# Optimization experiments

Hardware: AMD Instinct MI355X
Metric: run time of the kernel (lower is better)

## Reference

```python
import jax, jax.numpy as jnp
import numpy as np

B, N, C = 2, 2048, 1024
H = 16
HD = C // H  # 64


def setup_inputs() -> dict:
    key = jax.random.key(0)
    k1, k2, k3 = jax.random.split(key, 3)
    x = jax.random.normal(k1, (B, N, C), dtype=jnp.float32)
    w_qkv = jax.random.normal(k2, (C, 3 * C), dtype=jnp.float32) * (C ** -0.5)
    b_qkv = jnp.zeros((3 * C,), dtype=jnp.float32)
    w_out = jax.random.normal(k3, (C, C), dtype=jnp.float32) * (C ** -0.5)
    b_out = jnp.zeros((C,), dtype=jnp.float32)
    return {"x": x, "w_qkv": w_qkv, "b_qkv": b_qkv, "w_out": w_out, "b_out": b_out}


def reference(x, w_qkv, b_qkv, w_out, b_out):
    scale = HD ** -0.5
    # QKV projection: (B,N,3C) -> (B,N,3,H,HD) -> (B,3,H,N,HD)
    qkv = (jnp.einsum('bnc,cd->bnd', x, w_qkv) + b_qkv)
    qkv = qkv.reshape(B, N, 3, H, HD).transpose(0, 2, 3, 1, 4)
    q, k, v = qkv[:, 0], qkv[:, 1], qkv[:, 2]  # each (B,H,N,HD)
    # scaled dot-product attention with full NxN matrix (as in source)
    attn = jnp.einsum('bhnd,bhmd->bhnm', q, k) * scale
    attn = jax.nn.softmax(attn, axis=-1)
    out = jnp.einsum('bhnm,bhmd->bhnd', attn, v)  # (B,H,N,HD)
    out = out.transpose(0, 2, 1, 3).reshape(B, N, C)
    out = jnp.einsum('bnc,cd->bnd', out, w_out) + b_out
    return out
```

## Files before the change

### kernel.cpp

```cpp
#include <hip/hip_runtime.h>
#include <stdint.h>

using uint = unsigned int;
using ushort = unsigned short;

constexpr int Bb = 2;
constexpr int Ns = 2048;
constexpr int Cd = 1024;
constexpr int Hh = 16;
constexpr int HD = 64;
constexpr int BHND = Bb * Hh * Ns * HD;

typedef __attribute__((ext_vector_type(8))) short short8;
typedef __attribute__((ext_vector_type(4))) float floatx4;

__device__ inline ushort f2bf(float f) {
  uint u = __float_as_uint(f);
  return (ushort)((u + 0x7fffu + ((u >> 16) & 1u)) >> 16);
}
__device__ inline ushort f2bfr(float f) {
  return (ushort)((__float_as_uint(f) + 0x8000u) >> 16);
}

__global__ __launch_bounds__(256) void cvt_f32_bf16(
    const float* __restrict__ in, ushort* __restrict__ outp) {
  const int i = blockIdx.x * 256 + threadIdx.x;
  const float4 v = ((const float4*)in)[i];
  ushort4 o;
  o.x = f2bf(v.x); o.y = f2bf(v.y); o.z = f2bf(v.z); o.w = f2bf(v.w);
  ((ushort4*)outp)[i] = o;
}

__global__ __launch_bounds__(256) void transpose_f32_bf16(
    const float* __restrict__ in, ushort* __restrict__ outp, int R, int Cc) {
  __shared__ alignas(16) ushort tile[32][33];
  const int c0 = blockIdx.x * 32, r0 = blockIdx.y * 32;
  const int tx = threadIdx.x & 31;
  const int ty = threadIdx.x >> 5;
#pragma unroll
  for (int i = 0; i < 4; ++i)
    tile[ty + 8 * i][tx] = f2bf(in[(size_t)(r0 + ty + 8 * i) * Cc + c0 + tx]);
  __syncthreads();
#pragma unroll
  for (int i = 0; i < 4; ++i)
    outp[(size_t)(c0 + ty + 8 * i) * R + r0 + tx] = tile[tx][ty + 8 * i];
}

template <int MODE>
__global__ __launch_bounds__(256) void gemm_bt(
    const ushort* __restrict__ A, const ushort* __restrict__ Bt,
    const float* __restrict__ bias, void* __restrict__ outp,
    int M, int K, int Nn) {
  constexpr int LDT = 40;
  __shared__ alignas(16) ushort As[128 * LDT];
  __shared__ alignas(16) ushort Bs[128 * LDT];
  const int tid = threadIdx.x;
  const int wave = tid >> 6, lane = tid & 63;
  const int quad = lane >> 4, l16 = lane & 15;
  const int wr = wave >> 1, wc = wave & 1;
  const int m0 = blockIdx.x * 128, n0 = blockIdx.y * 128;

  const int srow0 = tid >> 2;
  const int skc = (tid & 3) * 8;

  const ushort* pa = A + (size_t)(m0 + srow0) * K + skc;
  const ushort* pb = Bt + (size_t)(n0 + srow0) * K + skc;

  floatx4 acc[4][4];
#pragma unroll
  for (int i = 0; i < 4; ++i)
#pragma unroll
    for (int j = 0; j < 4; ++j) {
      acc[i][j][0] = 0.f; acc[i][j][1] = 0.f; acc[i][j][2] = 0.f; acc[i][j][3] = 0.f;
    }

  uint4 ra0 = *(const uint4*)(pa);
  uint4 ra1 = *(const uint4*)(pa + (size_t)64 * K);
  uint4 rb0 = *(const uint4*)(pb);
  uint4 rb1 = *(const uint4*)(pb + (size_t)64 * K);

  const int nkt = K >> 5;
  for (int kt = 0; kt < nkt; ++kt) {
    __syncthreads();
    *(uint4*)&As[srow0 * LDT + skc] = ra0;
    *(uint4*)&As[(srow0 + 64) * LDT + skc] = ra1;
    *(uint4*)&Bs[srow0 * LDT + skc] = rb0;
    *(uint4*)&Bs[(srow0 + 64) * LDT + skc] = rb1;
    __syncthreads();
    if (kt + 1 < nkt) {
      const ushort* qa = pa + (size_t)(kt + 1) * 32;
      const ushort* qb = pb + (size_t)(kt + 1) * 32;
      ra0 = *(const uint4*)(qa);
      ra1 = *(const uint4*)(qa + (size_t)64 * K);
      rb0 = *(const uint4*)(qb);
      rb1 = *(const uint4*)(qb + (size_t)64 * K);
    }
    short8 af[4], bfv[4];
#pragma unroll
    for (int mt = 0; mt < 4; ++mt)
      af[mt] = *(const short8*)&As[(wr * 64 + mt * 16 + l16) * LDT + quad * 8];
#pragma unroll
    for (int nt = 0; nt < 4; ++nt)
      bfv[nt] = *(const short8*)&Bs[(wc * 64 + nt * 16 + l16) * LDT + quad * 8];
#pragma unroll
    for (int mt = 0; mt < 4; ++mt)
#pragma unroll
      for (int nt = 0; nt < 4; ++nt)
        acc[mt][nt] = __builtin_amdgcn_mfma_f32_16x16x32_bf16(af[mt], bfv[nt],
                                                              acc[mt][nt], 0, 0, 0);
  }

  if (MODE == 0) {
    ushort* qp = (ushort*)outp;
    ushort* kp = qp + BHND;
    ushort* vp = qp + 2 * BHND;
#pragma unroll
    for (int nt = 0; nt < 4; ++nt) {
      const int gn = n0 + wc * 64 + nt * 16 + l16;
      const float bv = bias[gn];
      const int which = gn >> 10, cc = gn & 1023;
      const int h = cc >> 6, d = cc & 63;
#pragma unroll
      for (int mt = 0; mt < 4; ++mt) {
#pragma unroll
        for (int r = 0; r < 4; ++r) {
          const int gm = m0 + wr * 64 + mt * 16 + quad * 4 + r;
          const int b = gm >> 11, n = gm & 2047;
          const ushort o = f2bfr(acc[mt][nt][r] + bv);
          const int bh = b * Hh + h;
          if (which == 0)
            qp[((size_t)bh * Ns + n) * HD + d] = o;
          else if (which == 1)
            kp[((size_t)bh * Ns + n) * HD + d] = o;
          else
            vp[((size_t)bh * HD + d) * Ns + n] = o;
        }
      }
    }
  } else {
    float* fout = (float*)outp;
#pragma unroll
    for (int nt = 0; nt < 4; ++nt) {
      const int gn = n0 + wc * 64 + nt * 16 + l16;
      const float bv = bias[gn];
#pragma unroll
      for (int mt = 0; mt < 4; ++mt)
#pragma unroll
        for (int r = 0; r < 4; ++r) {
          const int gm = m0 + wr * 64 + mt * 16 + quad * 4 + r;
          fout[(size_t)gm * Nn + gn] = acc[mt][nt][r] + bv;
        }
    }
  }
}

__global__ __launch_bounds__(256, 2) void attn(
    const ushort* __restrict__ q, const ushort* __restrict__ k,
    const ushort* __restrict__ vT, ushort* __restrict__ aout) {
  constexpr int LDK = 72;
  __shared__ alignas(16) ushort Ks[64 * LDK];
  __shared__ alignas(16) ushort Vs[64 * LDK];
  const int tid = threadIdx.x;
  const int wave = tid >> 6, lane = tid & 63;
  const int quad = lane >> 4, l16 = lane & 15;
  const int bh = blockIdx.y;
  const int qw = blockIdx.x * 128 + wave * 32;

  const ushort* kb = k + (size_t)bh * Ns * HD;
  const ushort* vb = vT + (size_t)bh * HD * Ns;

  short8 aq[2][2];
#pragma unroll
  for (int nqi = 0; nqi < 2; ++nqi) {
    const ushort* qp = q + ((size_t)bh * Ns + qw + nqi * 16 + l16) * HD + quad * 8;
    aq[nqi][0] = *(const short8*)(qp);
    aq[nqi][1] = *(const short8*)(qp + 32);
  }

  floatx4 accO[4][2];
#pragma unroll
  for (int mt = 0; mt < 4; ++mt)
#pragma unroll
    for (int nqi = 0; nqi < 2; ++nqi) {
      accO[mt][nqi][0] = 0.f; accO[mt][nqi][1] = 0.f;
      accO[mt][nqi][2] = 0.f; accO[mt][nqi][3] = 0.f;
    }
  float lst[2] = {0.f, 0.f};

  const int srow = tid >> 2;
  const int g0 = (tid & 3) * 2;
  const int cbA = (g0 >> 2) * 8 + ((g0 >> 1) & 1);
  const int g1 = g0 + 1;
  const int cbB = (g1 >> 2) * 8 + 4 + ((g1 >> 1) & 1);

  const ushort* kgp = kb + (size_t)srow * HD + g0 * 8;
  const ushort* vgp = vb + (size_t)srow * Ns + g0 * 8;
  ushort* ksw = &Ks[srow * LDK + g0 * 8];
  ushort* vswA = &Vs[srow * LDK + cbA * 4];
  ushort* vswB = &Vs[srow * LDK + cbB * 4];

  uint4 kg0 = *(const uint4*)(kgp);
  uint4 kg1 = *(const uint4*)(kgp + 8);
  uint4 vg0 = *(const uint4*)(vgp);
  uint4 vg1 = *(const uint4*)(vgp + 8);

  for (int kv0 = 0; kv0 < Ns; kv0 += 64) {
    __syncthreads();
    *(uint4*)ksw = kg0;
    *(uint4*)(ksw + 8) = kg1;
    *(uint2*)vswA = make_uint2(vg0.x, vg0.y);
    *(uint2*)(vswA + 8) = make_uint2(vg0.z, vg0.w);
    *(uint2*)vswB = make_uint2(vg1.x, vg1.y);
    *(uint2*)(vswB + 8) = make_uint2(vg1.z, vg1.w);
    __syncthreads();

    short8 ak[4][2], av[4][2];
#pragma unroll
    for (int t4 = 0; t4 < 4; ++t4) {
      const int ro = (t4 * 16 + l16) * LDK + quad * 8;
      ak[t4][0] = *(const short8*)&Ks[ro];
      ak[t4][1] = *(const short8*)&Ks[ro + 32];
      av[t4][0] = *(const short8*)&Vs[ro];
      av[t4][1] = *(const short8*)&Vs[ro + 32];
    }
    if (kv0 + 64 < Ns) {
      kg0 = *(const uint4*)(kgp + (size_t)(kv0 + 64) * HD);
      kg1 = *(const uint4*)(kgp + (size_t)(kv0 + 64) * HD + 8);
      vg0 = *(const uint4*)(vgp + kv0 + 64);
      vg1 = *(const uint4*)(vgp + kv0 + 64 + 8);
    }

#pragma unroll
    for (int nqi = 0; nqi < 2; ++nqi) {
      floatx4 sacc[4];
#pragma unroll
      for (int kvt = 0; kvt < 4; ++kvt) {
        sacc[kvt][0] = 0.f; sacc[kvt][1] = 0.f;
        sacc[kvt][2] = 0.f; sacc[kvt][3] = 0.f;
      }
#pragma unroll
      for (int kd = 0; kd < 2; ++kd)
#pragma unroll
        for (int kvt = 0; kvt < 4; ++kvt)
          sacc[kvt] = __builtin_amdgcn_mfma_f32_16x16x32_bf16(
              ak[kvt][kd], aq[nqi][kd], sacc[kvt], 0, 0, 0);

      uint ul[4], uh[4];
      float ls = 0.f;
#pragma unroll
      for (int kvt = 0; kvt < 4; ++kvt) {
        const float p0 = exp2f(sacc[kvt][0] * 0.18033688f);
        const float p1 = exp2f(sacc[kvt][1] * 0.18033688f);
        const float p2 = exp2f(sacc[kvt][2] * 0.18033688f);
        const float p3 = exp2f(sacc[kvt][3] * 0.18033688f);
        ls += (p0 + p1) + (p2 + p3);
        ul[kvt] = __builtin_amdgcn_perm(__float_as_uint(p1) + 0x8000u,
                                        __float_as_uint(p0) + 0x8000u, 0x07060302u);
        uh[kvt] = __builtin_amdgcn_perm(__float_as_uint(p3) + 0x8000u,
                                        __float_as_uint(p2) + 0x8000u, 0x07060302u);
      }
      lst[nqi] += ls;

#pragma unroll
      for (int ks = 0; ks < 2; ++ks) {
        union { uint u[4]; short8 s; } pf;
        pf.u[0] = ul[2 * ks]; pf.u[1] = uh[2 * ks];
        pf.u[2] = ul[2 * ks + 1]; pf.u[3] = uh[2 * ks + 1];
#pragma unroll
        for (int mt = 0; mt < 4; ++mt)
          accO[mt][nqi] = __builtin_amdgcn_mfma_f32_16x16x32_bf16(
              av[mt][ks], pf.s, accO[mt][nqi], 0, 0, 0);
      }
    }
  }

  const int b = bh >> 4, h = bh & 15;
#pragma unroll
  for (int nqi = 0; nqi < 2; ++nqi) {
    float l = lst[nqi];
    l += __shfl_xor(l, 16, 64);
    l += __shfl_xor(l, 32, 64);
    const float inv = 1.f / l;
    const int n = qw + nqi * 16 + l16;
#pragma unroll
    for (int mt = 0; mt < 4; ++mt) {
      ushort4 o;
      o.x = f2bfr(accO[mt][nqi][0] * inv);
      o.y = f2bfr(accO[mt][nqi][1] * inv);
      o.z = f2bfr(accO[mt][nqi][2] * inv);
      o.w = f2bfr(accO[mt][nqi][3] * inv);
      *(ushort4*)&aout[((size_t)(b * Ns + n)) * Cd + h * HD + mt * 16 + quad * 4] = o;
    }
  }
}

extern "C" void kernel_launch(void* const* d_in, const int* in_sizes, int n_in,
                              void* d_out, int out_size, void* d_ws, size_t ws_size,
                              hipStream_t stream) {
  (void)in_sizes; (void)n_in; (void)out_size; (void)ws_size;
  const float* x = (const float*)d_in[0];
  const float* w_qkv = (const float*)d_in[1];
  const float* b_qkv = (const float*)d_in[2];
  const float* w_out = (const float*)d_in[3];
  const float* b_out = (const float*)d_in[4];

  ushort* xbf = (ushort*)d_ws;
  ushort* wqkvT = xbf + (size_t)BHND;
  ushort* woutT = wqkvT + 3072 * 1024;
  ushort* qkvbuf = woutT + 1024 * 1024;
  ushort* aout = qkvbuf + 3 * (size_t)BHND;

  cvt_f32_bf16<<<dim3(BHND / 1024), 256, 0, stream>>>(x, xbf);
  transpose_f32_bf16<<<dim3(96, 32), 256, 0, stream>>>(w_qkv, wqkvT, 1024, 3072);
  transpose_f32_bf16<<<dim3(32, 32), 256, 0, stream>>>(w_out, woutT, 1024, 1024);

  gemm_bt<0><<<dim3(32, 24), 256, 0, stream>>>(xbf, wqkvT, b_qkv, qkvbuf,
                                               4096, 1024, 3072);
  attn<<<dim3(16, 32), 256, 0, stream>>>(qkvbuf, qkvbuf + BHND,
                                         qkvbuf + 2 * (size_t)BHND, aout);
  gemm_bt<1><<<dim3(32, 8), 256, 0, stream>>>(aout, woutT, b_out, d_out,
                                              4096, 1024, 1024);
}
```

Measured before the change: 208.2 us.

## Load K/V attention fragments directly from global into double-buffered registers

The attention kernel no longer stages K and V tiles through shared memory with two barriers per iteration. Each wave now loads its MFMA operand fragments straight from global memory into a two-slot register buffer, prefetching the next tile while computing the current one. To keep V fragments contiguous per lane, the QKV projection epilogue writes V^T with a permuted sequence index that reproduces the interleaving the old shared-memory write pattern produced. In exchange, each of the four waves fetches the full K/V tile from L2 itself, so cache traffic is multiplied. The doubled register arrays indexed by a runtime `cur` toggle also risk higher register pressure or scratch spills.

```diff
diff --git a/kernel.cpp b/kernel.cpp
--- a/kernel.cpp
+++ b/kernel.cpp
@@ -132,8 +132,10 @@
             qp[((size_t)bh * Ns + n) * HD + d] = o;
           else if (which == 1)
             kp[((size_t)bh * Ns + n) * HD + d] = o;
-          else
-            vp[((size_t)bh * HD + d) * Ns + n] = o;
+          else {
+            const int np = (n & ~28) | ((n & 12) << 1) | ((n & 16) >> 2);
+            vp[((size_t)bh * HD + d) * Ns + np] = o;
+          }
         }
       }
     }
@@ -157,9 +159,6 @@
 __global__ __launch_bounds__(256, 2) void attn(
     const ushort* __restrict__ q, const ushort* __restrict__ k,
     const ushort* __restrict__ vT, ushort* __restrict__ aout) {
-  constexpr int LDK = 72;
-  __shared__ alignas(16) ushort Ks[64 * LDK];
-  __shared__ alignas(16) ushort Vs[64 * LDK];
   const int tid = threadIdx.x;
   const int wave = tid >> 6, lane = tid & 63;
   const int quad = lane >> 4, l16 = lane & 15;
@@ -187,47 +186,36 @@
     }
   float lst[2] = {0.f, 0.f};
 
-  const int srow = tid >> 2;
-  const int g0 = (tid & 3) * 2;
-  const int cbA = (g0 >> 2) * 8 + ((g0 >> 1) & 1);
-  const int g1 = g0 + 1;
-  const int cbB = (g1 >> 2) * 8 + 4 + ((g1 >> 1) & 1);
-
-  const ushort* kgp = kb + (size_t)srow * HD + g0 * 8;
-  const ushort* vgp = vb + (size_t)srow * Ns + g0 * 8;
-  ushort* ksw = &Ks[srow * LDK + g0 * 8];
-  ushort* vswA = &Vs[srow * LDK + cbA * 4];
-  ushort* vswB = &Vs[srow * LDK + cbB * 4];
-
-  uint4 kg0 = *(const uint4*)(kgp);
-  uint4 kg1 = *(const uint4*)(kgp + 8);
-  uint4 vg0 = *(const uint4*)(vgp);
-  uint4 vg1 = *(const uint4*)(vgp + 8);
-
-  for (int kv0 = 0; kv0 < Ns; kv0 += 64) {
-    __syncthreads();
-    *(uint4*)ksw = kg0;
-    *(uint4*)(ksw + 8) = kg1;
-    *(uint2*)vswA = make_uint2(vg0.x, vg0.y);
-    *(uint2*)(vswA + 8) = make_uint2(vg0.z, vg0.w);
-    *(uint2*)vswB = make_uint2(vg1.x, vg1.y);
-    *(uint2*)(vswB + 8) = make_uint2(vg1.z, vg1.w);
-    __syncthreads();
-
-    short8 ak[4][2], av[4][2];
-#pragma unroll
-    for (int t4 = 0; t4 < 4; ++t4) {
-      const int ro = (t4 * 16 + l16) * LDK + quad * 8;
-      ak[t4][0] = *(const short8*)&Ks[ro];
-      ak[t4][1] = *(const short8*)&Ks[ro + 32];
-      av[t4][0] = *(const short8*)&Vs[ro];
-      av[t4][1] = *(const short8*)&Vs[ro + 32];
-    }
+  const ushort* kfp = kb + (size_t)l16 * HD + quad * 8;
+  const ushort* vfp = vb + (size_t)l16 * Ns + quad * 8;
+
+  short8 ak[2][4][2], av[2][4][2];
+#pragma unroll
+  for (int kvt = 0; kvt < 4; ++kvt)
+#pragma unroll
+    for (int kd = 0; kd < 2; ++kd)
+      ak[0][kvt][kd] = *(const short8*)(kfp + (size_t)kvt * 16 * HD + kd * 32);
+#pragma unroll
+  for (int mt = 0; mt < 4; ++mt)
+#pragma unroll
+    for (int ks = 0; ks < 2; ++ks)
+      av[0][mt][ks] = *(const short8*)(vfp + (size_t)mt * 16 * Ns + ks * 32);
+
+  int cur = 0;
+  for (int kv0 = 0; kv0 < Ns; kv0 += 64, cur ^= 1) {
     if (kv0 + 64 < Ns) {
-      kg0 = *(const uint4*)(kgp + (size_t)(kv0 + 64) * HD);
-      kg1 = *(const uint4*)(kgp + (size_t)(kv0 + 64) * HD + 8);
-      vg0 = *(const uint4*)(vgp + kv0 + 64);
-      vg1 = *(const uint4*)(vgp + kv0 + 64 + 8);
+      const ushort* kn = kfp + (size_t)(kv0 + 64) * HD;
+      const ushort* vn = vfp + (kv0 + 64);
+#pragma unroll
+      for (int kvt = 0; kvt < 4; ++kvt)
+#pragma unroll
+        for (int kd = 0; kd < 2; ++kd)
+          ak[cur ^ 1][kvt][kd] = *(const short8*)(kn + (size_t)kvt * 16 * HD + kd * 32);
+#pragma unroll
+      for (int mt = 0; mt < 4; ++mt)
+#pragma unroll
+        for (int ks = 0; ks < 2; ++ks)
+          av[cur ^ 1][mt][ks] = *(const short8*)(vn + (size_t)mt * 16 * Ns + ks * 32);
     }
 
 #pragma unroll
@@ -243,7 +231,7 @@
 #pragma unroll
         for (int kvt = 0; kvt < 4; ++kvt)
           sacc[kvt] = __builtin_amdgcn_mfma_f32_16x16x32_bf16(
-              ak[kvt][kd], aq[nqi][kd], sacc[kvt], 0, 0, 0);
+              ak[cur][kvt][kd], aq[nqi][kd], sacc[kvt], 0, 0, 0);
 
       uint ul[4], uh[4];
       float ls = 0.f;
@@ -269,7 +257,7 @@
 #pragma unroll
         for (int mt = 0; mt < 4; ++mt)
           accO[mt][nqi] = __builtin_amdgcn_mfma_f32_16x16x32_bf16(
-              av[mt][ks], pf.s, accO[mt][nqi], 0, 0, 0);
+              av[cur][mt][ks], pf.s, accO[mt][nqi], 0, 0, 0);
       }
     }
   }
```

Result: slower. 481.9 us (+131.4%).
